# Performance work log

Hardware: AMD Instinct MI355X
Metric: run time of the kernel (lower is better)

## Reference

```python
import jax, jax.numpy as jnp
import numpy as np

N = 16      # hparams.length (utterances)
T = 128     # tokens per utterance
D = 256     # local_feature_dim
DG = 256    # global_attention.input_dim
ATT = 128   # attention inner dim
R1 = 2 * N * N  # rgcn num_relations
H1 = 256    # rgcn.dim
H2 = 256    # gcn.dim
NEG = -1e9


def setup_inputs() -> dict:
    ks = jax.random.split(jax.random.key(0), 16)
    s = 0.02
    return {
        "global_features": jax.random.normal(ks[0], (N, DG), jnp.float32),
        "local_features": jax.random.normal(ks[1], (N, T, D), jnp.float32),
        "speaker": jax.random.randint(ks[2], (N,), 0, 2),
        "length": jax.random.randint(ks[3], (N,), 1, T + 1),
        # Bahdanau global attention params
        "Wq": jax.random.normal(ks[4], (DG, ATT), jnp.float32) * s,
        "Wk": jax.random.normal(ks[5], (DG, ATT), jnp.float32) * s,
        "v_att": jax.random.normal(ks[6], (ATT,), jnp.float32) * s,
        # Bidirectional local attention params
        "Wb1": jax.random.normal(ks[7], (D, ATT), jnp.float32) * s,
        "Wb2": jax.random.normal(ks[8], (D, ATT), jnp.float32) * s,
        # RGCN layer 1 (2*N^2 relations)
        "Wrel1": jax.random.normal(ks[9], (R1, D, H1), jnp.float32) * s,
        "Wroot1": jax.random.normal(ks[10], (D, H1), jnp.float32) * s,
        "b1": jnp.zeros((H1,), jnp.float32),
        # RGCN layer 2 (1 relation)
        "Wrel2": jax.random.normal(ks[11], (1, H1, H2), jnp.float32) * s,
        "Wroot2": jax.random.normal(ks[12], (H1, H2), jnp.float32) * s,
        "b2": jnp.zeros((H2,), jnp.float32),
    }


def _rgcn_fg(x, Wrel, Wroot, b, e_src, e_dst, rel, ew, n_nodes):
    # x: [N,T,din], ew: [E,Ts,Td] (src-token x dst-token weights), Wrel: [R,din,dout]
    We = Wrel[rel]                 # [E,din,dout] irregular gather over relations
    xs = x[e_src]                  # [E,T,din]
    # message aligned with dst tokens: sum over src tokens t -> dst token s
    msg = jnp.einsum('ets,etd,edo->eso', ew, xs, We)   # [E,T,dout]
    agg = jax.ops.segment_sum(msg, e_dst, num_segments=n_nodes)
    return agg + x @ Wroot + b


def reference(global_features, local_features, speaker, length,
              Wq, Wk, v_att, Wb1, Wb2,
              Wrel1, Wroot1, b1, Wrel2, Wroot2, b2):
    n = global_features.shape[0]
    t = local_features.shape[1]

    # --- Bahdanau global attention: query i over keys j ---
    q = global_features @ Wq                         # [N,A]
    k = global_features @ Wk                         # [N,A]
    s = jnp.tanh(q[:, None, :] + k[None, :, :]) @ v_att   # [N,N]
    gw = jax.nn.softmax(s, axis=1).reshape(-1)       # [N*N]

    # --- Bidirectional local attention, vectorized over all (i,j) pairs ---
    p1 = local_features @ Wb1                        # [N,T,A]
    p2 = local_features @ Wb2                        # [N,T,A]
    S = jnp.einsum('ita,jsa->ijts', p1, p2)          # [N,N,T,T]
    pos = jnp.arange(t)
    valid = pos[None, :] < length[:, None]           # [N,T]
    S = jnp.where(valid[None, :, None, :], S, NEG)   # mask key tokens of j
    w1 = jax.nn.softmax(S, axis=-1)                  # softmax over j's tokens
    w1 = w1 * valid[:, None, :, None]                # zero padded query rows of i
    lw = w1.reshape(n * n, t, t)                     # [E,T,T]

    # --- edge weights & relation ids ---
    ew1 = gw[:, None, None] * lw                     # [E,T,T]
    e_src = jnp.arange(n * n) // n                   # edge (i,j): src=i
    e_dst = jnp.arange(n * n) % n                    # dst=j
    direction = jnp.where(e_src < e_dst, 0, 1)
    rel = (speaker[e_src] * n + speaker[e_dst]) * 2 + direction

    # --- two attention-weighted relational GCN layers ---
    x1 = _rgcn_fg(local_features, Wrel1, Wroot1, b1, e_src, e_dst, rel, ew1, n)
    x2 = _rgcn_fg(x1, Wrel2, Wroot2, b2, e_src, e_dst, jnp.zeros_like(rel), lw, n)
    return x2
```

## Files before the change

### kernel.cpp

```cpp
#include <hip/hip_runtime.h>

#define NODES 16
#define TT    128
#define DIM   256
#define ATTD  128
#define HD    256
#define NEGV  -1e9f

typedef short bf16x8 __attribute__((ext_vector_type(8)));
typedef float f32x4  __attribute__((ext_vector_type(4)));
typedef unsigned short ushort_t;
typedef ushort_t u16x4 __attribute__((ext_vector_type(4)));
typedef ushort_t u16x8 __attribute__((ext_vector_type(8)));

__device__ __forceinline__ ushort_t f2b(float f) {
  union { float f; unsigned u; } v; v.f = f;
  unsigned r = (v.u + 0x7fffu + ((v.u >> 16) & 1u)) >> 16;
  return (ushort_t)r;
}
__device__ __forceinline__ float b2f(ushort_t h) {
  union { unsigned u; float f; } v; v.u = ((unsigned)h) << 16; return v.f;
}

__device__ __forceinline__ void wave_gemm_step(const ushort_t* __restrict__ A, int as, int R0,
                                               const ushort_t* __restrict__ BT, int bs, int C0,
                                               int kb, int lr, f32x4 acc[4][4]) {
  bf16x8 a[4], b[4];
#pragma unroll
  for (int m = 0; m < 4; ++m)
    a[m] = *(const bf16x8*)(A + (size_t)(R0 + m * 16 + lr) * as + kb);
#pragma unroll
  for (int n = 0; n < 4; ++n)
    b[n] = *(const bf16x8*)(BT + (size_t)(C0 + n * 16 + lr) * bs + kb);
#pragma unroll
  for (int m = 0; m < 4; ++m)
#pragma unroll
    for (int n = 0; n < 4; ++n)
      acc[m][n] = __builtin_amdgcn_mfma_f32_16x16x32_bf16(a[m], b[n], acc[m][n], 0, 0, 0);
}

#define WAVE_SETUP                                    \
  int tid = threadIdx.x;                              \
  int wave = tid >> 6, lane = tid & 63;               \
  int wr = wave >> 1, wc = wave & 1;                  \
  int lr = lane & 15, kg = lane >> 4;                 \
  (void)wr; (void)wc;

#define ACC_INIT(acc)                                 \
  f32x4 acc[4][4];                                    \
  { f32x4 z = {0.f, 0.f, 0.f, 0.f};                   \
    _Pragma("unroll") for (int m = 0; m < 4; ++m)     \
    _Pragma("unroll") for (int n = 0; n < 4; ++n) acc[m][n] = z; }

template <int ROWB>
__device__ __forceinline__ void stage_tileN(const ushort_t* __restrict__ src,
                                            ushort_t* __restrict__ dst, int tid) {
  constexpr int CPR = ROWB / 16;
  constexpr int PASSES = 128 * CPR / 256;
#pragma unroll
  for (int p = 0; p < PASSES; ++p) {
    int idx = p * 256 + tid;
    int row = idx / CPR;
    int cb  = (idx % CPR) << 4;
    u16x8 v = *(const u16x8*)(src + (size_t)row * (ROWB / 2) + (cb >> 1));
    *(u16x8*)((char*)dst + row * ROWB + (cb ^ ((row & 7) << 4))) = v;
  }
}

template <int ROWB>
__device__ __forceinline__ void lds_gemmN(const ushort_t* __restrict__ A,
                                          const ushort_t* __restrict__ B,
                                          int R0, int C0, int lr, int kg,
                                          f32x4 acc[4][4]) {
#pragma unroll
  for (int kk = 0; kk < ROWB / 64; ++kk) {
    int cb = kk * 64 + kg * 16;
    bf16x8 a[4], b[4];
#pragma unroll
    for (int m = 0; m < 4; ++m) {
      int row = R0 + m * 16 + lr;
      a[m] = *(const bf16x8*)((const char*)A + row * ROWB + (cb ^ ((row & 7) << 4)));
    }
#pragma unroll
    for (int n = 0; n < 4; ++n) {
      int row = C0 + n * 16 + lr;
      b[n] = *(const bf16x8*)((const char*)B + row * ROWB + (cb ^ ((row & 7) << 4)));
    }
#pragma unroll
    for (int m = 0; m < 4; ++m)
#pragma unroll
      for (int n = 0; n < 4; ++n)
        acc[m][n] = __builtin_amdgcn_mfma_f32_16x16x32_bf16(a[m], b[n], acc[m][n], 0, 0, 0);
  }
}

__global__ void k_prep(const float* __restrict__ Lf, ushort_t* __restrict__ Lfh,
                       const float* __restrict__ Wb1, const float* __restrict__ Wb2,
                       const float* __restrict__ Wroot1, const float* __restrict__ Wroot2,
                       const float* __restrict__ Wrel2, const float* __restrict__ Wrel1,
                       ushort_t* __restrict__ Wb1T, ushort_t* __restrict__ Wb2T,
                       ushort_t* __restrict__ Wroot1T, ushort_t* __restrict__ Wroot2T,
                       ushort_t* __restrict__ Wrel2T, ushort_t* __restrict__ Wrel1T8,
                       const float* __restrict__ G, const float* __restrict__ Wq,
                       const float* __restrict__ Wk, float* __restrict__ qk) {
  int blk = blockIdx.x;
  if (blk < 256) {
    int gi = blk * 256 + threadIdx.x;
    const float4* src = (const float4*)Lf;
    float4 v0 = src[gi * 2], v1 = src[gi * 2 + 1];
    u16x8 o;
    o[0] = f2b(v0.x); o[1] = f2b(v0.y); o[2] = f2b(v0.z); o[3] = f2b(v0.w);
    o[4] = f2b(v1.x); o[5] = f2b(v1.y); o[6] = f2b(v1.z); o[7] = f2b(v1.w);
    *(u16x8*)(Lfh + (size_t)gi * 8) = o;
  } else if (blk < 448) {
    __shared__ float lds[64][65];
    int b = blk - 256;
    const float* src; ushort_t* dst; int R, C, t;
    if (b < 8)       { src = Wb1;    dst = Wb1T;    R = 256; C = 128; t = b; }
    else if (b < 16) { src = Wb2;    dst = Wb2T;    R = 256; C = 128; t = b - 8; }
    else if (b < 32) { src = Wroot1; dst = Wroot1T; R = 256; C = 256; t = b - 16; }
    else if (b < 48) { src = Wroot2; dst = Wroot2T; R = 256; C = 256; t = b - 32; }
    else if (b < 64) { src = Wrel2;  dst = Wrel2T;  R = 256; C = 256; t = b - 48; }
    else {
      int m = (b - 64) >> 4;
      int relid = (m >> 2) * 32 + (m & 3);
      src = Wrel1 + (size_t)relid * 65536;
      dst = Wrel1T8 + (size_t)m * 65536;
      R = 256; C = 256; t = (b - 64) & 15;
    }
    int tilesC = C >> 6;
    int r0 = (t / tilesC) * 64, c0 = (t % tilesC) * 64;
    int tid = threadIdx.x;
    for (int p = 0; p < 16; ++p) {
      int idx = p * 256 + tid, rr = idx >> 6, cc = idx & 63;
      lds[rr][cc] = src[(size_t)(r0 + rr) * C + c0 + cc];
    }
    __syncthreads();
    for (int p = 0; p < 16; ++p) {
      int idx = p * 256 + tid, rr = idx >> 6, cc = idx & 63;
      dst[(size_t)(c0 + rr) * R + r0 + cc] = f2b(lds[cc][rr]);
    }
  } else {
    int i = blk - 448, t = threadIdx.x;
    const float* W = (t < 128) ? Wq : Wk;
    int a = t & 127;
    float acc = 0.f;
#pragma unroll 8
    for (int d = 0; d < DIM; ++d)
      acc = fmaf(G[i * DIM + d], W[d * ATTD + a], acc);
    int dst = (t < 128) ? i : (NODES + i);
    qk[(size_t)dst * ATTD + a] = acc;
  }
}

__global__ __launch_bounds__(256, 1)
void k_phaseB(const float* __restrict__ qk, const float* __restrict__ vatt,
              float* __restrict__ gw,
              const ushort_t* __restrict__ Lfh,
              const ushort_t* __restrict__ Wb1T, const ushort_t* __restrict__ Wb2T,
              ushort_t* __restrict__ p1h, ushort_t* __restrict__ p2h,
              const ushort_t* __restrict__ Wroot1T, const float* __restrict__ b1,
              float* __restrict__ x1part,
              const ushort_t* __restrict__ Wrel1T8, const int* __restrict__ spk,
              ushort_t* __restrict__ YT) {
  __shared__ ushort_t sA[32768];
  __shared__ ushort_t sB[32768];
  int blk = blockIdx.x;
  if (blk < 16) {
    __shared__ float sred[NODES][17];
    __shared__ float q[ATTD];
    int i = blk, t = threadIdx.x;
    int j = t >> 4, ag = t & 15;
    if (t < ATTD) q[t] = qk[(size_t)i * ATTD + t];
    __syncthreads();
    float sum = 0.f;
#pragma unroll
    for (int u = 0; u < 8; ++u) {
      int a = ag * 8 + u;
      sum += tanhf(q[a] + qk[(size_t)(NODES + j) * ATTD + a]) * vatt[a];
    }
    sred[j][ag] = sum;
    __syncthreads();
    if (t < NODES) {
      float s = 0.f;
#pragma unroll
      for (int u = 0; u < 16; ++u) s += sred[t][u];
      sred[t][16] = s;
    }
    __syncthreads();
    if (t == 0) {
      float m = -1e30f;
      for (int jj = 0; jj < NODES; ++jj) m = fmaxf(m, sred[jj][16]);
      float ex[NODES], ssum = 0.f;
      for (int jj = 0; jj < NODES; ++jj) { ex[jj] = __expf(sred[jj][16] - m); ssum += ex[jj]; }
      float inv = 1.f / ssum;
      for (int jj = 0; jj < NODES; ++jj) gw[i * NODES + jj] = ex[jj] * inv;
    }
  } else if (blk < 48) {
    int t = blk - 16;
    int sel = t >> 4, bx = t & 15;
    const ushort_t* BT = sel ? Wb2T : Wb1T;
    ushort_t* out = sel ? p2h : p1h;
    WAVE_SETUP
    stage_tileN<512>(Lfh + (size_t)bx * 128 * DIM, sA, tid);
    stage_tileN<512>(BT, sB, tid);
    __syncthreads();
    ACC_INIT(acc)
    lds_gemmN<512>(sA, sB, wr * 64, wc * 64, lr, kg, acc);
    int R0 = bx * 128 + wr * 64, C0 = wc * 64;
#pragma unroll
    for (int m = 0; m < 4; ++m)
#pragma unroll
      for (int n = 0; n < 4; ++n) {
        int col = C0 + n * 16 + lr;
#pragma unroll
        for (int r = 0; r < 4; ++r) {
          int row = R0 + m * 16 + kg * 4 + r;
          out[(size_t)row * ATTD + col] = f2b(acc[m][n][r]);
        }
      }
  } else if (blk < 80) {
    int t = blk - 48;
    int bx = t & 15, by = t >> 4;
    WAVE_SETUP
    stage_tileN<512>(Lfh + (size_t)bx * 128 * DIM, sA, tid);
    stage_tileN<512>(Wroot1T + (size_t)by * 128 * DIM, sB, tid);
    __syncthreads();
    ACC_INIT(acc)
    lds_gemmN<512>(sA, sB, wr * 64, wc * 64, lr, kg, acc);
    int R0 = bx * 128 + wr * 64, C0 = by * 128 + wc * 64;
#pragma unroll
    for (int m = 0; m < 4; ++m)
#pragma unroll
      for (int n = 0; n < 4; ++n) {
        int col = C0 + n * 16 + lr;
        float bb = b1[col];
#pragma unroll
        for (int r = 0; r < 4; ++r) {
          int row = R0 + m * 16 + kg * 4 + r;
          x1part[(size_t)row * HD + col] = acc[m][n][r] + bb;
        }
      }
  } else {
    int t = blk - 80;
    int iq = t >> 1, cy = t & 1;
    int i = iq >> 2, q = iq & 3;
    int m8 = spk[i] * 4 + q;
    WAVE_SETUP
    stage_tileN<512>(Lfh + (size_t)i * TT * DIM, sA, tid);
    stage_tileN<512>(Wrel1T8 + (size_t)m8 * 65536 + (size_t)cy * 128 * DIM, sB, tid);
    __syncthreads();
    ACC_INIT(acc)
    lds_gemmN<512>(sA, sB, wr * 64, wc * 64, lr, kg, acc);
    int R0 = wr * 64, C0 = cy * 128 + wc * 64;
#pragma unroll
    for (int m = 0; m < 4; ++m)
#pragma unroll
      for (int n = 0; n < 4; ++n) {
        int o = C0 + n * 16 + lr;
        int t0 = R0 + m * 16 + kg * 4;
        u16x4 v;
#pragma unroll
        for (int r = 0; r < 4; ++r) v[r] = f2b(acc[m][n][r]);
        *(u16x4*)(YT + (size_t)iq * 32768 + (size_t)o * TT + t0) = v;
      }
  }
}

__global__ __launch_bounds__(256, 1)
void k_locatt(const ushort_t* __restrict__ p1h, const ushort_t* __restrict__ p2h,
              const int* __restrict__ length,
              ushort_t* __restrict__ lwT) {
  __shared__ ushort_t sA[16384];
  __shared__ ushort_t sB[16384];
  __shared__ float S[TT][129];
  __shared__ float red[TT][2];
  __shared__ float sInv[TT];
  int e = blockIdx.x, i = e >> 4, j = e & 15;
  WAVE_SETUP
  int R0 = wr * 64, C0 = wc * 64;
  stage_tileN<256>(p1h + (size_t)i * TT * ATTD, sA, tid);
  stage_tileN<256>(p2h + (size_t)j * TT * ATTD, sB, tid);
  __syncthreads();
  ACC_INIT(acc)
  lds_gemmN<256>(sA, sB, R0, C0, lr, kg, acc);
#pragma unroll
  for (int m = 0; m < 4; ++m)
#pragma unroll
    for (int n = 0; n < 4; ++n)
#pragma unroll
      for (int r = 0; r < 4; ++r)
        S[R0 + m * 16 + kg * 4 + r][C0 + n * 16 + lr] = acc[m][n][r];
  __syncthreads();
  int leni = length[i], lenj = length[j];
  int t = tid & 127, h = tid >> 7, s0 = h * 64;
  float mx = -1e30f;
  for (int s = s0; s < s0 + 64; ++s) {
    float vv = (s < lenj) ? S[t][s] : NEGV;
    mx = fmaxf(mx, vv);
  }
  red[t][h] = mx;
  __syncthreads();
  mx = fmaxf(red[t][0], red[t][1]);
  __syncthreads();
  float sum = 0.f;
  for (int s = s0; s < s0 + 64; ++s) {
    float vv = (s < lenj) ? S[t][s] : NEGV;
    float ee = __expf(vv - mx);
    S[t][s] = ee;
    sum += ee;
  }
  red[t][h] = sum;
  __syncthreads();
  if (h == 0) sInv[t] = (t < leni) ? 1.f / (red[t][0] + red[t][1]) : 0.f;
  __syncthreads();
  int s = tid >> 1;
  int t0 = (tid & 1) * 64;
  size_t base = (size_t)e * 16384 + (size_t)s * TT;
  for (int tb = 0; tb < 64; tb += 8) {
    u16x8 w;
#pragma unroll
    for (int u = 0; u < 8; ++u) {
      int tt = t0 + tb + u;
      w[u] = f2b(S[tt][s] * sInv[tt]);
    }
    *(u16x8*)(lwT + base + t0 + tb) = w;
  }
}

__global__ __launch_bounds__(256, 1)
void k_wagg(const ushort_t* __restrict__ lwT, const ushort_t* __restrict__ Bsrc,
            const float* __restrict__ gw, const int* __restrict__ spk,
            ushort_t* __restrict__ partH, int mode) {
  __shared__ ushort_t lds[4][16384];
  int g = blockIdx.x, j = blockIdx.y, oh = blockIdx.z;
  WAVE_SETUP
  int R0 = wr * 64, C0 = wc * 64;
  int i0 = g * 2, i1 = g * 2 + 1;
  int e0 = i0 * NODES + j, e1 = i1 * NODES + j;
  const ushort_t* B0;
  const ushort_t* B1;
  float ge0, ge1;
  if (mode == 1) {
    int q0 = spk[j] * 2 + ((i0 < j) ? 0 : 1);
    int q1 = spk[j] * 2 + ((i1 < j) ? 0 : 1);
    B0 = Bsrc + (size_t)(i0 * 4 + q0) * 32768 + (size_t)oh * 16384;
    B1 = Bsrc + (size_t)(i1 * 4 + q1) * 32768 + (size_t)oh * 16384;
    ge0 = gw[e0]; ge1 = gw[e1];
  } else {
    B0 = Bsrc + (size_t)i0 * 32768 + (size_t)oh * 16384;
    B1 = Bsrc + (size_t)i1 * 32768 + (size_t)oh * 16384;
    ge0 = 1.f; ge1 = 1.f;
  }
  stage_tileN<256>(lwT + (size_t)e0 * 16384, lds[0], tid);
  stage_tileN<256>(B0, lds[1], tid);
  __syncthreads();
  stage_tileN<256>(lwT + (size_t)e1 * 16384, lds[2], tid);
  stage_tileN<256>(B1, lds[3], tid);
  ACC_INIT(acc0)
  lds_gemmN<256>(lds[0], lds[1], R0, C0, lr, kg, acc0);
  __syncthreads();
  ACC_INIT(acc1)
  lds_gemmN<256>(lds[2], lds[3], R0, C0, lr, kg, acc1);
  size_t base = (size_t)(g * NODES + j) * TT * HD + (size_t)oh * 128;
#pragma unroll
  for (int m = 0; m < 4; ++m)
#pragma unroll
    for (int n = 0; n < 4; ++n) {
      int ocol = C0 + n * 16 + lr;
#pragma unroll
      for (int r = 0; r < 4; ++r) {
        int s = R0 + m * 16 + kg * 4 + r;
        partH[base + (size_t)s * HD + ocol] = f2b(ge0 * acc0[m][n][r] + ge1 * acc1[m][n][r]);
      }
    }
}

__global__ __launch_bounds__(256, 1)
void k_reduce1(const ushort_t* __restrict__ partH, const float* __restrict__ x1part,
               ushort_t* __restrict__ x1h, ushort_t* __restrict__ x1T) {
  __shared__ ushort_t L[TT][40];
  int j = blockIdx.x, oc0 = blockIdx.y * 32, tid = threadIdx.x;
  const size_t Q = (size_t)NODES * TT * HD;
#pragma unroll
  for (int p = 0; p < 4; ++p) {
    int idx = p * 256 + tid;
    int t = idx >> 3, o4 = (idx & 7) * 4;
    size_t goff = ((size_t)j * TT + t) * HD + oc0 + o4;
    float4 s = *(const float4*)(x1part + goff);
#pragma unroll
    for (int g = 0; g < 8; ++g) {
      u16x4 pv = *(const u16x4*)(partH + (size_t)g * Q + goff);
      s.x += b2f(pv[0]); s.y += b2f(pv[1]); s.z += b2f(pv[2]); s.w += b2f(pv[3]);
    }
    u16x4 hv; hv[0] = f2b(s.x); hv[1] = f2b(s.y); hv[2] = f2b(s.z); hv[3] = f2b(s.w);
    *(u16x4*)(x1h + goff) = hv;
    *(u16x4*)(&L[t][o4]) = hv;
  }
  __syncthreads();
#pragma unroll
  for (int p = 0; p < 2; ++p) {
    int idx = p * 256 + tid;
    int o = idx >> 4, t8 = (idx & 15) * 8;
    u16x8 v;
#pragma unroll
    for (int u = 0; u < 8; ++u) v[u] = L[t8 + u][o];
    *(u16x8*)(x1T + (size_t)j * 32768 + (size_t)(oc0 + o) * TT + t8) = v;
  }
}

__global__ void k_reduce2(const ushort_t* __restrict__ partH, ushort_t* __restrict__ Z2h) {
  int idx = blockIdx.x * 256 + threadIdx.x;
  size_t o4 = (size_t)idx * 4;
  const size_t Q = (size_t)NODES * TT * HD;
  float4 s = {0.f, 0.f, 0.f, 0.f};
#pragma unroll
  for (int g = 0; g < 8; ++g) {
    u16x4 pv = *(const u16x4*)(partH + (size_t)g * Q + o4);
    s.x += b2f(pv[0]); s.y += b2f(pv[1]); s.z += b2f(pv[2]); s.w += b2f(pv[3]);
  }
  u16x4 hv; hv[0] = f2b(s.x); hv[1] = f2b(s.y); hv[2] = f2b(s.z); hv[3] = f2b(s.w);
  *(u16x4*)(Z2h + o4) = hv;
}

__global__ __launch_bounds__(64, 1)
void k_final(const ushort_t* __restrict__ Z2h, const ushort_t* __restrict__ Wrel2T,
             const ushort_t* __restrict__ x1h, const ushort_t* __restrict__ Wroot2T,
             const float* __restrict__ b2, float* __restrict__ out) {
  int lane = threadIdx.x;
  int lr = lane & 15, kg = lane >> 4;
  int R0 = blockIdx.x * 64, C0 = blockIdx.y * 64;
  ACC_INIT(acc)
  for (int kk = 0; kk < 8; ++kk)
    wave_gemm_step(Z2h, HD, R0, Wrel2T, HD, C0, kk * 32 + kg * 8, lr, acc);
  for (int kk = 0; kk < 8; ++kk)
    wave_gemm_step(x1h, HD, R0, Wroot2T, HD, C0, kk * 32 + kg * 8, lr, acc);
#pragma unroll
  for (int m = 0; m < 4; ++m)
#pragma unroll
    for (int n = 0; n < 4; ++n) {
      int col = C0 + n * 16 + lr;
      float bb = b2[col];
#pragma unroll
      for (int r = 0; r < 4; ++r) {
        int row = R0 + m * 16 + kg * 4 + r;
        out[(size_t)row * HD + col] = acc[m][n][r] + bb;
      }
    }
}

extern "C" void kernel_launch(void* const* d_in, const int* in_sizes, int n_in,
                              void* d_out, int out_size, void* d_ws, size_t ws_size,
                              hipStream_t stream) {
  (void)in_sizes; (void)n_in; (void)out_size; (void)ws_size;
  const float* G      = (const float*)d_in[0];
  const float* Lf     = (const float*)d_in[1];
  const int*   spk    = (const int*)d_in[2];
  const int*   len    = (const int*)d_in[3];
  const float* Wq     = (const float*)d_in[4];
  const float* Wk     = (const float*)d_in[5];
  const float* vatt   = (const float*)d_in[6];
  const float* Wb1    = (const float*)d_in[7];
  const float* Wb2    = (const float*)d_in[8];
  const float* Wrel1  = (const float*)d_in[9];
  const float* Wroot1 = (const float*)d_in[10];
  const float* b1     = (const float*)d_in[11];
  const float* Wrel2  = (const float*)d_in[12];
  const float* Wroot2 = (const float*)d_in[13];
  const float* b2     = (const float*)d_in[14];

  char* ws = (char*)d_ws;
  const size_t MB = 1ull << 20;
  float*    gw      = (float*)(ws);
  float*    qk      = (float*)(ws + 16 * 1024);
  ushort_t* Lfh     = (ushort_t*)(ws + 1 * MB);
  ushort_t* Wb1T    = (ushort_t*)(ws + 2 * MB);
  ushort_t* Wb2T    = (ushort_t*)(ws + 2 * MB + 64 * 1024);
  ushort_t* Wroot1T = (ushort_t*)(ws + 2 * MB + 128 * 1024);
  ushort_t* Wroot2T = (ushort_t*)(ws + 2 * MB + 256 * 1024);
  ushort_t* Wrel2T  = (ushort_t*)(ws + 2 * MB + 384 * 1024);
  ushort_t* Wrel1T8 = (ushort_t*)(ws + 2 * MB + 512 * 1024);
  ushort_t* p1h     = (ushort_t*)(ws + 4 * MB);
  ushort_t* p2h     = (ushort_t*)(ws + 4 * MB + 512 * 1024);
  ushort_t* lwT     = (ushort_t*)(ws + 5 * MB);
  ushort_t* YT      = (ushort_t*)(ws + 21 * MB);
  float*    x1part  = (float*)(ws + 25 * MB);
  ushort_t* partH   = (ushort_t*)(ws + 27 * MB);
  ushort_t* x1h     = (ushort_t*)(ws + 43 * MB);
  ushort_t* x1T     = (ushort_t*)(ws + 44 * MB);
  ushort_t* Z2h     = (ushort_t*)(ws + 45 * MB);
  float* out = (float*)d_out;

  k_prep<<<464, 256, 0, stream>>>(Lf, Lfh, Wb1, Wb2, Wroot1, Wroot2, Wrel2, Wrel1,
                                  Wb1T, Wb2T, Wroot1T, Wroot2T, Wrel2T, Wrel1T8,
                                  G, Wq, Wk, qk);
  k_phaseB<<<208, 256, 0, stream>>>(qk, vatt, gw, Lfh, Wb1T, Wb2T, p1h, p2h,
                                    Wroot1T, b1, x1part, Wrel1T8, spk, YT);
  k_locatt<<<256, 256, 0, stream>>>(p1h, p2h, len, lwT);
  k_wagg<<<dim3(8, 16, 2), 256, 0, stream>>>(lwT, YT, gw, spk, partH, 1);
  k_reduce1<<<dim3(16, 8), 256, 0, stream>>>(partH, x1part, x1h, x1T);
  k_wagg<<<dim3(8, 16, 2), 256, 0, stream>>>(lwT, x1T, gw, spk, partH, 2);
  k_reduce2<<<512, 256, 0, stream>>>(partH, Z2h);
  k_final<<<dim3(32, 4), 64, 0, stream>>>(Z2h, Wrel2T, x1h, Wroot2T, b2, out);
}
```

Measured before the change: 73.64 us.

## Double-buffer LDS staging in K-halves across GEMM kernels and split final GEMM

Replaces whole-tile LDS staging with 64-column K chunks staged into two alternating buffers, so global loads of the next chunk overlap MFMA work on the current one in phaseB, locatt and wagg. LDS footprint shrinks through unions and the smaller buffers, which may allow more blocks per CU. k_final now computes narrower 64x32 tiles with twice as many blocks to raise parallelism. The cost is more barriers and chunk-loop overhead.

```diff
diff --git a/kernel.cpp b/kernel.cpp
--- a/kernel.cpp
+++ b/kernel.cpp
@@ -52,39 +52,35 @@
     _Pragma("unroll") for (int m = 0; m < 4; ++m)     \
     _Pragma("unroll") for (int n = 0; n < 4; ++n) acc[m][n] = z; }
 
-template <int ROWB>
-__device__ __forceinline__ void stage_tileN(const ushort_t* __restrict__ src,
-                                            ushort_t* __restrict__ dst, int tid) {
-  constexpr int CPR = ROWB / 16;
-  constexpr int PASSES = 128 * CPR / 256;
-#pragma unroll
-  for (int p = 0; p < PASSES; ++p) {
+__device__ __forceinline__ void stage_half(const ushort_t* __restrict__ src, int srcs,
+                                           ushort_t* __restrict__ dst, int tid) {
+#pragma unroll
+  for (int p = 0; p < 4; ++p) {
     int idx = p * 256 + tid;
-    int row = idx / CPR;
-    int cb  = (idx % CPR) << 4;
-    u16x8 v = *(const u16x8*)(src + (size_t)row * (ROWB / 2) + (cb >> 1));
-    *(u16x8*)((char*)dst + row * ROWB + (cb ^ ((row & 7) << 4))) = v;
-  }
-}
-
-template <int ROWB>
-__device__ __forceinline__ void lds_gemmN(const ushort_t* __restrict__ A,
-                                          const ushort_t* __restrict__ B,
+    int row = idx >> 3;
+    int cb  = (idx & 7) << 4;
+    u16x8 v = *(const u16x8*)(src + (size_t)row * srcs + (cb >> 1));
+    *(u16x8*)((char*)dst + row * 128 + (cb ^ ((row & 7) << 4))) = v;
+  }
+}
+
+__device__ __forceinline__ void gemm_half(const ushort_t* __restrict__ bufA,
+                                          const ushort_t* __restrict__ bufB,
                                           int R0, int C0, int lr, int kg,
                                           f32x4 acc[4][4]) {
 #pragma unroll
-  for (int kk = 0; kk < ROWB / 64; ++kk) {
+  for (int kk = 0; kk < 2; ++kk) {
     int cb = kk * 64 + kg * 16;
     bf16x8 a[4], b[4];
 #pragma unroll
     for (int m = 0; m < 4; ++m) {
       int row = R0 + m * 16 + lr;
-      a[m] = *(const bf16x8*)((const char*)A + row * ROWB + (cb ^ ((row & 7) << 4)));
+      a[m] = *(const bf16x8*)((const char*)bufA + row * 128 + (cb ^ ((row & 7) << 4)));
     }
 #pragma unroll
     for (int n = 0; n < 4; ++n) {
       int row = C0 + n * 16 + lr;
-      b[n] = *(const bf16x8*)((const char*)B + row * ROWB + (cb ^ ((row & 7) << 4)));
+      b[n] = *(const bf16x8*)((const char*)bufB + row * 128 + (cb ^ ((row & 7) << 4)));
     }
 #pragma unroll
     for (int m = 0; m < 4; ++m)
@@ -115,18 +111,18 @@
   } else if (blk < 448) {
     __shared__ float lds[64][65];
     int b = blk - 256;
-    const float* src; ushort_t* dst; int R, C, t;
-    if (b < 8)       { src = Wb1;    dst = Wb1T;    R = 256; C = 128; t = b; }
-    else if (b < 16) { src = Wb2;    dst = Wb2T;    R = 256; C = 128; t = b - 8; }
-    else if (b < 32) { src = Wroot1; dst = Wroot1T; R = 256; C = 256; t = b - 16; }
-    else if (b < 48) { src = Wroot2; dst = Wroot2T; R = 256; C = 256; t = b - 32; }
-    else if (b < 64) { src = Wrel2;  dst = Wrel2T;  R = 256; C = 256; t = b - 48; }
+    const float* src; ushort_t* dst; int C, t;
+    if (b < 8)       { src = Wb1;    dst = Wb1T;    C = 128; t = b; }
+    else if (b < 16) { src = Wb2;    dst = Wb2T;    C = 128; t = b - 8; }
+    else if (b < 32) { src = Wroot1; dst = Wroot1T; C = 256; t = b - 16; }
+    else if (b < 48) { src = Wroot2; dst = Wroot2T; C = 256; t = b - 32; }
+    else if (b < 64) { src = Wrel2;  dst = Wrel2T;  C = 256; t = b - 48; }
     else {
       int m = (b - 64) >> 4;
       int relid = (m >> 2) * 32 + (m & 3);
       src = Wrel1 + (size_t)relid * 65536;
       dst = Wrel1T8 + (size_t)m * 65536;
-      R = 256; C = 256; t = (b - 64) & 15;
+      C = 256; t = (b - 64) & 15;
     }
     int tilesC = C >> 6;
     int r0 = (t / tilesC) * 64, c0 = (t % tilesC) * 64;
@@ -138,7 +134,7 @@
     __syncthreads();
     for (int p = 0; p < 16; ++p) {
       int idx = p * 256 + tid, rr = idx >> 6, cc = idx & 63;
-      dst[(size_t)(c0 + rr) * R + r0 + cc] = f2b(lds[cc][rr]);
+      dst[(size_t)(c0 + rr) * 256 + r0 + cc] = f2b(lds[cc][rr]);
     }
   } else {
     int i = blk - 448, t = threadIdx.x;
@@ -163,50 +159,72 @@
               float* __restrict__ x1part,
               const ushort_t* __restrict__ Wrel1T8, const int* __restrict__ spk,
               ushort_t* __restrict__ YT) {
-  __shared__ ushort_t sA[32768];
-  __shared__ ushort_t sB[32768];
+  __shared__ union {
+    ushort_t buf[2][16384];
+    struct { float sred[NODES][17]; float q[ATTD]; } sc;
+  } sh;
   int blk = blockIdx.x;
   if (blk < 16) {
-    __shared__ float sred[NODES][17];
-    __shared__ float q[ATTD];
     int i = blk, t = threadIdx.x;
     int j = t >> 4, ag = t & 15;
-    if (t < ATTD) q[t] = qk[(size_t)i * ATTD + t];
+    if (t < ATTD) sh.sc.q[t] = qk[(size_t)i * ATTD + t];
     __syncthreads();
     float sum = 0.f;
 #pragma unroll
     for (int u = 0; u < 8; ++u) {
       int a = ag * 8 + u;
-      sum += tanhf(q[a] + qk[(size_t)(NODES + j) * ATTD + a]) * vatt[a];
-    }
-    sred[j][ag] = sum;
+      sum += tanhf(sh.sc.q[a] + qk[(size_t)(NODES + j) * ATTD + a]) * vatt[a];
+    }
+    sh.sc.sred[j][ag] = sum;
     __syncthreads();
     if (t < NODES) {
       float s = 0.f;
 #pragma unroll
-      for (int u = 0; u < 16; ++u) s += sred[t][u];
-      sred[t][16] = s;
+      for (int u = 0; u < 16; ++u) s += sh.sc.sred[t][u];
+      sh.sc.sred[t][16] = s;
     }
     __syncthreads();
     if (t == 0) {
       float m = -1e30f;
-      for (int jj = 0; jj < NODES; ++jj) m = fmaxf(m, sred[jj][16]);
+      for (int jj = 0; jj < NODES; ++jj) m = fmaxf(m, sh.sc.sred[jj][16]);
       float ex[NODES], ssum = 0.f;
-      for (int jj = 0; jj < NODES; ++jj) { ex[jj] = __expf(sred[jj][16] - m); ssum += ex[jj]; }
+      for (int jj = 0; jj < NODES; ++jj) { ex[jj] = __expf(sh.sc.sred[jj][16] - m); ssum += ex[jj]; }
       float inv = 1.f / ssum;
       for (int jj = 0; jj < NODES; ++jj) gw[i * NODES + jj] = ex[jj] * inv;
     }
-  } else if (blk < 48) {
-    int t = blk - 16;
-    int sel = t >> 4, bx = t & 15;
-    const ushort_t* BT = sel ? Wb2T : Wb1T;
+    return;
+  }
+  WAVE_SETUP
+  const ushort_t* Asrc; const ushort_t* Bsrc;
+  if (blk < 48) {
+    int t = blk - 16; int sel = t >> 4, bx = t & 15;
+    Asrc = Lfh + (size_t)bx * 128 * DIM;
+    Bsrc = sel ? Wb2T : Wb1T;
+  } else if (blk < 80) {
+    int t = blk - 48; int bx = t & 15, by = t >> 4;
+    Asrc = Lfh + (size_t)bx * 128 * DIM;
+    Bsrc = Wroot1T + (size_t)by * 128 * DIM;
+  } else {
+    int t = blk - 80; int iq = t >> 1, cy = t & 1;
+    int i = iq >> 2, q = iq & 3;
+    int m8 = spk[i] * 4 + q;
+    Asrc = Lfh + (size_t)i * TT * DIM;
+    Bsrc = Wrel1T8 + (size_t)m8 * 65536 + (size_t)cy * 128 * DIM;
+  }
+  stage_half(Asrc, DIM, sh.buf[0], tid);
+  stage_half(Bsrc, DIM, sh.buf[0] + 8192, tid);
+  __syncthreads();
+  ACC_INIT(acc)
+  for (int c = 1; c < 4; ++c) {
+    stage_half(Asrc + c * 64, DIM, sh.buf[c & 1], tid);
+    stage_half(Bsrc + c * 64, DIM, sh.buf[c & 1] + 8192, tid);
+    gemm_half(sh.buf[(c & 1) ^ 1], sh.buf[(c & 1) ^ 1] + 8192, wr * 64, wc * 64, lr, kg, acc);
+    __syncthreads();
+  }
+  gemm_half(sh.buf[1], sh.buf[1] + 8192, wr * 64, wc * 64, lr, kg, acc);
+  if (blk < 48) {
+    int t = blk - 16; int sel = t >> 4, bx = t & 15;
     ushort_t* out = sel ? p2h : p1h;
-    WAVE_SETUP
-    stage_tileN<512>(Lfh + (size_t)bx * 128 * DIM, sA, tid);
-    stage_tileN<512>(BT, sB, tid);
-    __syncthreads();
-    ACC_INIT(acc)
-    lds_gemmN<512>(sA, sB, wr * 64, wc * 64, lr, kg, acc);
     int R0 = bx * 128 + wr * 64, C0 = wc * 64;
 #pragma unroll
     for (int m = 0; m < 4; ++m)
@@ -220,14 +238,7 @@
         }
       }
   } else if (blk < 80) {
-    int t = blk - 48;
-    int bx = t & 15, by = t >> 4;
-    WAVE_SETUP
-    stage_tileN<512>(Lfh + (size_t)bx * 128 * DIM, sA, tid);
-    stage_tileN<512>(Wroot1T + (size_t)by * 128 * DIM, sB, tid);
-    __syncthreads();
-    ACC_INIT(acc)
-    lds_gemmN<512>(sA, sB, wr * 64, wc * 64, lr, kg, acc);
+    int t = blk - 48; int bx = t & 15, by = t >> 4;
     int R0 = bx * 128 + wr * 64, C0 = by * 128 + wc * 64;
 #pragma unroll
     for (int m = 0; m < 4; ++m)
@@ -242,16 +253,7 @@
         }
       }
   } else {
-    int t = blk - 80;
-    int iq = t >> 1, cy = t & 1;
-    int i = iq >> 2, q = iq & 3;
-    int m8 = spk[i] * 4 + q;
-    WAVE_SETUP
-    stage_tileN<512>(Lfh + (size_t)i * TT * DIM, sA, tid);
-    stage_tileN<512>(Wrel1T8 + (size_t)m8 * 65536 + (size_t)cy * 128 * DIM, sB, tid);
-    __syncthreads();
-    ACC_INIT(acc)
-    lds_gemmN<512>(sA, sB, wr * 64, wc * 64, lr, kg, acc);
+    int t = blk - 80; int iq = t >> 1, cy = t & 1;
     int R0 = wr * 64, C0 = cy * 128 + wc * 64;
 #pragma unroll
     for (int m = 0; m < 4; ++m)
@@ -271,32 +273,40 @@
 void k_locatt(const ushort_t* __restrict__ p1h, const ushort_t* __restrict__ p2h,
               const int* __restrict__ length,
               ushort_t* __restrict__ lwT) {
-  __shared__ ushort_t sA[16384];
-  __shared__ ushort_t sB[16384];
-  __shared__ float S[TT][129];
+  __shared__ union {
+    ushort_t buf[2][16384];
+    float S[TT][129];
+  } sh;
   __shared__ float red[TT][2];
   __shared__ float sInv[TT];
   int e = blockIdx.x, i = e >> 4, j = e & 15;
   WAVE_SETUP
   int R0 = wr * 64, C0 = wc * 64;
-  stage_tileN<256>(p1h + (size_t)i * TT * ATTD, sA, tid);
-  stage_tileN<256>(p2h + (size_t)j * TT * ATTD, sB, tid);
-  __syncthreads();
+  const ushort_t* A = p1h + (size_t)i * TT * ATTD;
+  const ushort_t* B = p2h + (size_t)j * TT * ATTD;
+  stage_half(A, ATTD, sh.buf[0], tid);
+  stage_half(B, ATTD, sh.buf[0] + 8192, tid);
+  __syncthreads();
+  stage_half(A + 64, ATTD, sh.buf[1], tid);
+  stage_half(B + 64, ATTD, sh.buf[1] + 8192, tid);
   ACC_INIT(acc)
-  lds_gemmN<256>(sA, sB, R0, C0, lr, kg, acc);
+  gemm_half(sh.buf[0], sh.buf[0] + 8192, R0, C0, lr, kg, acc);
+  __syncthreads();
+  gemm_half(sh.buf[1], sh.buf[1] + 8192, R0, C0, lr, kg, acc);
+  __syncthreads();
 #pragma unroll
   for (int m = 0; m < 4; ++m)
 #pragma unroll
     for (int n = 0; n < 4; ++n)
 #pragma unroll
       for (int r = 0; r < 4; ++r)
-        S[R0 + m * 16 + kg * 4 + r][C0 + n * 16 + lr] = acc[m][n][r];
+        sh.S[R0 + m * 16 + kg * 4 + r][C0 + n * 16 + lr] = acc[m][n][r];
   __syncthreads();
   int leni = length[i], lenj = length[j];
   int t = tid & 127, h = tid >> 7, s0 = h * 64;
   float mx = -1e30f;
   for (int s = s0; s < s0 + 64; ++s) {
-    float vv = (s < lenj) ? S[t][s] : NEGV;
+    float vv = (s < lenj) ? sh.S[t][s] : NEGV;
     mx = fmaxf(mx, vv);
   }
   red[t][h] = mx;
@@ -305,9 +315,9 @@
   __syncthreads();
   float sum = 0.f;
   for (int s = s0; s < s0 + 64; ++s) {
-    float vv = (s < lenj) ? S[t][s] : NEGV;
+    float vv = (s < lenj) ? sh.S[t][s] : NEGV;
     float ee = __expf(vv - mx);
-    S[t][s] = ee;
+    sh.S[t][s] = ee;
     sum += ee;
   }
   red[t][h] = sum;
@@ -322,7 +332,7 @@
 #pragma unroll
     for (int u = 0; u < 8; ++u) {
       int tt = t0 + tb + u;
-      w[u] = f2b(S[tt][s] * sInv[tt]);
+      w[u] = f2b(sh.S[tt][s] * sInv[tt]);
     }
     *(u16x8*)(lwT + base + t0 + tb) = w;
   }
@@ -332,7 +342,7 @@
 void k_wagg(const ushort_t* __restrict__ lwT, const ushort_t* __restrict__ Bsrc,
             const float* __restrict__ gw, const int* __restrict__ spk,
             ushort_t* __restrict__ partH, int mode) {
-  __shared__ ushort_t lds[4][16384];
+  __shared__ ushort_t buf[2][16384];
   int g = blockIdx.x, j = blockIdx.y, oh = blockIdx.z;
   WAVE_SETUP
   int R0 = wr * 64, C0 = wc * 64;
@@ -352,16 +362,26 @@
     B1 = Bsrc + (size_t)i1 * 32768 + (size_t)oh * 16384;
     ge0 = 1.f; ge1 = 1.f;
   }
-  stage_tileN<256>(lwT + (size_t)e0 * 16384, lds[0], tid);
-  stage_tileN<256>(B0, lds[1], tid);
-  __syncthreads();
-  stage_tileN<256>(lwT + (size_t)e1 * 16384, lds[2], tid);
-  stage_tileN<256>(B1, lds[3], tid);
+  const ushort_t* A0 = lwT + (size_t)e0 * 16384;
+  const ushort_t* A1 = lwT + (size_t)e1 * 16384;
+  stage_half(A0, TT, buf[0], tid);
+  stage_half(B0, TT, buf[0] + 8192, tid);
+  __syncthreads();
+  stage_half(A0 + 64, TT, buf[1], tid);
+  stage_half(B0 + 64, TT, buf[1] + 8192, tid);
   ACC_INIT(acc0)
-  lds_gemmN<256>(lds[0], lds[1], R0, C0, lr, kg, acc0);
-  __syncthreads();
+  gemm_half(buf[0], buf[0] + 8192, R0, C0, lr, kg, acc0);
+  __syncthreads();
+  stage_half(A1, TT, buf[0], tid);
+  stage_half(B1, TT, buf[0] + 8192, tid);
+  gemm_half(buf[1], buf[1] + 8192, R0, C0, lr, kg, acc0);
+  __syncthreads();
+  stage_half(A1 + 64, TT, buf[1], tid);
+  stage_half(B1 + 64, TT, buf[1] + 8192, tid);
   ACC_INIT(acc1)
-  lds_gemmN<256>(lds[2], lds[3], R0, C0, lr, kg, acc1);
+  gemm_half(buf[0], buf[0] + 8192, R0, C0, lr, kg, acc1);
+  __syncthreads();
+  gemm_half(buf[1], buf[1] + 8192, R0, C0, lr, kg, acc1);
   size_t base = (size_t)(g * NODES + j) * TT * HD + (size_t)oh * 128;
 #pragma unroll
   for (int m = 0; m < 4; ++m)
@@ -429,16 +449,36 @@
              const float* __restrict__ b2, float* __restrict__ out) {
   int lane = threadIdx.x;
   int lr = lane & 15, kg = lane >> 4;
-  int R0 = blockIdx.x * 64, C0 = blockIdx.y * 64;
-  ACC_INIT(acc)
-  for (int kk = 0; kk < 8; ++kk)
-    wave_gemm_step(Z2h, HD, R0, Wrel2T, HD, C0, kk * 32 + kg * 8, lr, acc);
-  for (int kk = 0; kk < 8; ++kk)
-    wave_gemm_step(x1h, HD, R0, Wroot2T, HD, C0, kk * 32 + kg * 8, lr, acc);
+  int R0 = blockIdx.x * 64, C0 = blockIdx.y * 32;
+  f32x4 acc[4][2];
+  { f32x4 z = {0.f, 0.f, 0.f, 0.f};
+#pragma unroll
+    for (int m = 0; m < 4; ++m)
+#pragma unroll
+      for (int n = 0; n < 2; ++n) acc[m][n] = z; }
+  for (int src = 0; src < 2; ++src) {
+    const ushort_t* A  = src ? x1h : Z2h;
+    const ushort_t* BT = src ? Wroot2T : Wrel2T;
+    for (int kk = 0; kk < 8; ++kk) {
+      int kb = kk * 32 + kg * 8;
+      bf16x8 a[4], b[2];
+#pragma unroll
+      for (int m = 0; m < 4; ++m)
+        a[m] = *(const bf16x8*)(A + (size_t)(R0 + m * 16 + lr) * HD + kb);
+#pragma unroll
+      for (int n = 0; n < 2; ++n)
+        b[n] = *(const bf16x8*)(BT + (size_t)(C0 + n * 16 + lr) * HD + kb);
+#pragma unroll
+      for (int m = 0; m < 4; ++m)
+#pragma unroll
+        for (int n = 0; n < 2; ++n)
+          acc[m][n] = __builtin_amdgcn_mfma_f32_16x16x32_bf16(a[m], b[n], acc[m][n], 0, 0, 0);
+    }
+  }
 #pragma unroll
   for (int m = 0; m < 4; ++m)
 #pragma unroll
-    for (int n = 0; n < 4; ++n) {
+    for (int n = 0; n < 2; ++n) {
       int col = C0 + n * 16 + lr;
       float bb = b2[col];
 #pragma unroll
@@ -501,5 +541,5 @@
   k_reduce1<<<dim3(16, 8), 256, 0, stream>>>(partH, x1part, x1h, x1T);
   k_wagg<<<dim3(8, 16, 2), 256, 0, stream>>>(lwT, x1T, gw, spk, partH, 2);
   k_reduce2<<<512, 256, 0, stream>>>(partH, Z2h);
-  k_final<<<dim3(32, 4), 64, 0, stream>>>(Z2h, Wrel2T, x1h, Wroot2T, b2, out);
-}
+  k_final<<<dim3(32, 8), 64, 0, stream>>>(Z2h, Wrel2T, x1h, Wroot2T, b2, out);
+}
```

Result: no change. 73.54 us (-0.1%).
